# Optimization experiments

Hardware: AMD Instinct MI355X
Metric: run time of the kernel (lower is better)

The kernel has to match this reference:

```python
import jax, jax.numpy as jnp
import numpy as np

B, CH, H, W = 128, 3, 224, 224
R = 14
S = R * R  # 196 superpixels
DIMS = [11, 96, 192, 384, 768, 768]
BN_EPS = 1e-5


def setup_inputs() -> dict:
    key = jax.random.key(0)
    ks = jax.random.split(key, 64)
    inp = {}
    inp["x"] = jax.random.normal(ks[0], (B, CH, H, W), jnp.float32)
    inp["sliced"] = jax.random.randint(ks[1], (B, H, W), 0, S, jnp.int32)
    ki = 2
    for i in range(5):
        ci, co = DIMS[i], DIMS[i + 1]
        inp[f"w{i}"] = jax.random.normal(ks[ki], (co, ci), jnp.float32) / np.sqrt(ci); ki += 1
        inp[f"b{i}"] = jnp.zeros((co,), jnp.float32)
        inp[f"g{i}"] = jnp.ones((co,), jnp.float32)
        inp[f"be{i}"] = jnp.zeros((co,), jnp.float32)
        inp[f"rm{i}"] = jax.random.normal(ks[ki], (co,), jnp.float32) * 0.1; ki += 1
        inp[f"rv{i}"] = jax.random.uniform(ks[ki], (co,), jnp.float32) + 0.5; ki += 1
    return inp


def _seg_features(x, sliced):
    # x: [B,3,H,W] float, sliced: [B,H,W] int labels in [0,S)
    b, c, h, w = x.shape
    n = h * w
    ids = sliced.reshape(b, n).astype(jnp.int32)
    gid = (jnp.arange(b, dtype=jnp.int32)[:, None] * S + ids).reshape(-1)  # [B*N]

    counts = jax.ops.segment_sum(jnp.ones((b * n,), x.dtype), gid, num_segments=b * S)  # [B*S]
    rows = jnp.repeat(jnp.arange(h, dtype=x.dtype), w)
    cols = jnp.tile(jnp.arange(w, dtype=x.dtype), h)
    coords = jnp.stack([rows, cols], -1)                       # [N,2]
    coords_b = jnp.broadcast_to(coords, (b, n, 2)).reshape(b * n, 2)
    coord_sum = jax.ops.segment_sum(coords_b, gid, num_segments=b * S)  # [B*S,2]

    rgb = x.reshape(b, c, n).transpose(0, 2, 1).reshape(b * n, c)       # [B*N,3]
    rgb_sum = jax.ops.segment_sum(rgb, gid, num_segments=b * S)
    rgb_sq = jax.ops.segment_sum(rgb * rgb, gid, num_segments=b * S)

    cnt = counts[:, None]
    safe = jnp.maximum(cnt, 1.0)
    mean_coord = coord_sum / safe                              # [B*S,2]
    mean_rgb = rgb_sum / safe                                  # [B*S,3]
    # torch .std is unbiased; NaN (count<=1) replaced by 0
    var = (rgb_sq - cnt * mean_rgb * mean_rgb) / jnp.maximum(cnt - 1.0, 1.0)
    std = jnp.where(cnt > 1.0, jnp.sqrt(jnp.maximum(var, 0.0)), 0.0)

    mc = mean_coord.reshape(b, S, 2)
    mr = mean_rgb.reshape(b, S, 3)
    sd = std.reshape(b, S, 3)
    # gather pixel at the (truncated) mean location of each segment
    ri = jnp.clip(mc[..., 0].astype(jnp.int32), 0, h - 1)      # [B,S]
    ci = jnp.clip(mc[..., 1].astype(jnp.int32), 0, w - 1)
    gathered = x[jnp.arange(b)[:, None], :, ri, ci]            # [B,S,3]

    feat = jnp.concatenate([mc, mr, sd, gathered], -1)         # [B,S,11]
    feat = feat * (counts.reshape(b, S, 1) > 0).astype(x.dtype)  # absent segments stay 0
    return feat.transpose(0, 2, 1).reshape(b, 11, R, R)


def _conv_bn(h, w, b, g, be, rm, rv, act):
    # 1x1 conv == channel contraction
    h = jnp.einsum('bchw,oc->bohw', h, w) + b[None, :, None, None]
    scale = g / jnp.sqrt(rv + BN_EPS)
    h = (h - rm[None, :, None, None]) * scale[None, :, None, None] + be[None, :, None, None]
    return jax.nn.relu(h) if act else h


def reference(x, sliced,
              w0, b0, g0, be0, rm0, rv0,
              w1, b1, g1, be1, rm1, rv1,
              w2, b2, g2, be2, rm2, rv2,
              w3, b3, g3, be3, rm3, rv3,
              w4, b4, g4, be4, rm4, rv4):
    params = [(w0, b0, g0, be0, rm0, rv0), (w1, b1, g1, be1, rm1, rv1),
              (w2, b2, g2, be2, rm2, rv2), (w3, b3, g3, be3, rm3, rv3),
              (w4, b4, g4, be4, rm4, rv4)]
    h = _seg_features(x, sliced)                # [B,11,14,14]
    for i, (w, b, g, be, rm, rv) in enumerate(params):
        h = _conv_bn(h, w, b, g, be, rm, rv, act=(i < 4))  # last block: BN only
    return (sliced, h)
```

## Files before the change

kernel.cpp:

```cpp
#include <hip/hip_runtime.h>
#include <hip/hip_bf16.h>

#define HW    50176
#define IMGW  224
#define SEG   196
#define NBATCH 128
#define NCOL  (NBATCH * SEG)
#define PB    14
#define CHUNK (HW / PB)
#define VCHUNK (CHUNK / 4)

typedef __attribute__((ext_vector_type(8))) short bf16x8;
typedef __attribute__((ext_vector_type(4))) float f32x4;
typedef unsigned long long u64;

static __device__ __forceinline__ ushort f2bf(float v) {
    __hip_bfloat16 h = __float2bfloat16(v);
    return *reinterpret_cast<ushort*>(&h);
}

__global__ __launch_bounds__(256) void seg_accum(const float* __restrict__ x,
                                                 const int*   __restrict__ sl,
                                                 float*       __restrict__ stats,
                                                 float*       __restrict__ outf) {
    __shared__ u64 ls[4][SEG];
    int b    = blockIdx.x / PB;
    int part = blockIdx.x % PB;
    int tid  = threadIdx.x;

    for (int i = tid; i < 4 * SEG; i += 256) (&ls[0][0])[i] = 0ull;
    __syncthreads();

    const float* xb = x + (size_t)b * 3 * HW;
    const int*   sb = sl + (size_t)b * HW;
    float4*      ob = (float4*)(outf + (size_t)b * HW);
    int v0 = part * VCHUNK;

    for (int vi = tid; vi < VCHUNK; vi += 256) {
        int vg = v0 + vi;
        int4   id4 = ((const int4*)sb)[vg];
        float4 r4  = ((const float4*)xb)[vg];
        float4 g4  = ((const float4*)(xb + HW))[vg];
        float4 b4  = ((const float4*)(xb + 2 * HW))[vg];

        ob[vg] = make_float4((float)id4.x, (float)id4.y, (float)id4.z, (float)id4.w);

        int p   = vg * 4;
        int row = p / IMGW;
        int col = p - row * IMGW;
        u64 rowbits = ((u64)1 << 48) | ((u64)(unsigned)row << 24);

#pragma unroll
        for (int q = 0; q < 4; ++q) {
            int   id = (q == 0) ? id4.x : (q == 1) ? id4.y : (q == 2) ? id4.z : id4.w;
            float r  = (q == 0) ? r4.x  : (q == 1) ? r4.y  : (q == 2) ? r4.z  : r4.w;
            float g  = (q == 0) ? g4.x  : (q == 1) ? g4.y  : (q == 2) ? g4.z  : g4.w;
            float bl = (q == 0) ? b4.x  : (q == 1) ? b4.y  : (q == 2) ? b4.z  : b4.w;

            unsigned qr  = (unsigned)fmaf(r,  8192.f, 131072.5f);
            unsigned qg  = (unsigned)fmaf(g,  8192.f, 131072.5f);
            unsigned qb  = (unsigned)fmaf(bl, 8192.f, 131072.5f);
            unsigned qr2 = (unsigned)fmaf(r * r,  2048.f, 0.5f);
            unsigned qg2 = (unsigned)fmaf(g * g,  2048.f, 0.5f);
            unsigned qb2 = (unsigned)fmaf(bl * bl, 2048.f, 0.5f);

            atomicAdd(&ls[0][id], rowbits | (unsigned)(col + q));
            atomicAdd(&ls[1][id], ((u64)qg  << 32) | qr);
            atomicAdd(&ls[2][id], ((u64)qr2 << 32) | qb);
            atomicAdd(&ls[3][id], ((u64)qb2 << 32) | qg2);
        }
    }
    __syncthreads();

    const float inv_s = 1.f / 8192.f, inv_q = 1.f / 2048.f;
    for (int i = tid; i < SEG; i += 256) {
        u64 v0p = ls[0][i];
        unsigned cnt = (unsigned)(v0p >> 48);
        if (!cnt) continue;
        float fc   = (float)cnt;
        float rows = (float)((unsigned)(v0p >> 24) & 0xFFFFFFu);
        float cols = (float)((unsigned)v0p & 0xFFFFFFu);
        u64 v1 = ls[1][i], v2 = ls[2][i], v3 = ls[3][i];
        float bias = 16.f * fc;
        float rsum = (float)(unsigned)v1         * inv_s - bias;
        float gsum = (float)(unsigned)(v1 >> 32) * inv_s - bias;
        float bsum = (float)(unsigned)v2         * inv_s - bias;
        float rsq  = (float)(unsigned)(v2 >> 32) * inv_q;
        float gsq  = (float)(unsigned)v3         * inv_q;
        float bsq  = (float)(unsigned)(v3 >> 32) * inv_q;

        size_t base = (size_t)b * SEG + i;
        atomicAdd(&stats[0 * NCOL + base], fc);
        atomicAdd(&stats[1 * NCOL + base], rows);
        atomicAdd(&stats[2 * NCOL + base], cols);
        atomicAdd(&stats[3 * NCOL + base], rsum);
        atomicAdd(&stats[4 * NCOL + base], gsum);
        atomicAdd(&stats[5 * NCOL + base], bsum);
        atomicAdd(&stats[6 * NCOL + base], rsq);
        atomicAdd(&stats[7 * NCOL + base], gsq);
        atomicAdd(&stats[8 * NCOL + base], bsq);
    }
}

__global__ __launch_bounds__(256) void convert_all(
    const float* __restrict__ s0, const float* __restrict__ s1,
    const float* __restrict__ s2, const float* __restrict__ s3,
    const float* __restrict__ s4,
    ushort* __restrict__ d0, ushort* __restrict__ d1, ushort* __restrict__ d2,
    ushort* __restrict__ d3, ushort* __restrict__ d4) {
    int blk = blockIdx.x;
    const float* src; ushort* dst; int Cout, K, Kpad, base;
    if (blk < 32)        { src = s0; dst = d0; Cout = 96;  K = 11;  Kpad = 64;  base = 0;    }
    else if (blk < 160)  { src = s1; dst = d1; Cout = 192; K = 96;  Kpad = 128; base = 32;   }
    else if (blk < 544)  { src = s2; dst = d2; Cout = 384; K = 192; Kpad = 256; base = 160;  }
    else if (blk < 1696) { src = s3; dst = d3; Cout = 768; K = 384; Kpad = 384; base = 544;  }
    else                 { src = s4; dst = d4; Cout = 768; K = 768; Kpad = 768; base = 1696; }
    int i = (blk - base) * 256 + threadIdx.x;
    int o = i / Kpad, k = i - o * Kpad;
    float v = (o < Cout && k < K) ? src[(size_t)o * K + k] : 0.f;
    dst[i] = f2bf(v);
}

#define SH_W   0
#define SH_F   16384
#define SH_A0  20480
#define SH_A1  28672

__global__ __launch_bounds__(256) void fused_l012(
    const float* __restrict__ x,
    const float* __restrict__ stats,
    const ushort* __restrict__ W0g, const ushort* __restrict__ W1g, const ushort* __restrict__ W2g,
    const float* __restrict__ bias0, const float* __restrict__ gam0, const float* __restrict__ bet0,
    const float* __restrict__ rm0,  const float* __restrict__ rv0,
    const float* __restrict__ bias1, const float* __restrict__ gam1, const float* __restrict__ bet1,
    const float* __restrict__ rm1,  const float* __restrict__ rv1,
    const float* __restrict__ bias2, const float* __restrict__ gam2, const float* __restrict__ bet2,
    const float* __restrict__ rm2,  const float* __restrict__ rv2,
    ushort* __restrict__ outA)
{
    __shared__ ushort sh[45056];
    int tid  = threadIdx.x;
    int lane = tid & 63;
    int wid  = tid >> 6;
    int mrow = lane & 15;
    int quad = lane >> 4;
    int n0   = blockIdx.x * 64;

    if (tid < 64) {
        int r = tid, n = n0 + r;
        float cnt  = stats[n];
        float safe = fmaxf(cnt, 1.f);
        float inv  = 1.f / safe;
        float fmrow = stats[1 * NCOL + n] * inv;
        float fmcol = stats[2 * NCOL + n] * inv;
        float fmr   = stats[3 * NCOL + n] * inv;
        float fmg   = stats[4 * NCOL + n] * inv;
        float fmb   = stats[5 * NCOL + n] * inv;
        float den  = fmaxf(cnt - 1.f, 1.f);
        float vr = (stats[6 * NCOL + n] - cnt * fmr * fmr) / den;
        float vg = (stats[7 * NCOL + n] - cnt * fmg * fmg) / den;
        float vb = (stats[8 * NCOL + n] - cnt * fmb * fmb) / den;
        bool  has2 = cnt > 1.f;
        float sr = has2 ? sqrtf(fmaxf(vr, 0.f)) : 0.f;
        float sg = has2 ? sqrtf(fmaxf(vg, 0.f)) : 0.f;
        float sb = has2 ? sqrtf(fmaxf(vb, 0.f)) : 0.f;
        int b = n / SEG;
        int ri = min(max((int)fmrow, 0), IMGW - 1);
        int ci = min(max((int)fmcol, 0), IMGW - 1);
        const float* xb = x + (size_t)b * 3 * HW;
        int pi = ri * IMGW + ci;
        float gr = xb[pi], gg = xb[HW + pi], gb = xb[2 * HW + pi];
        float mask = cnt > 0.f ? 1.f : 0.f;

        int rx = r & 7;
        bf16x8 v0;
        v0[0] = (short)f2bf(fmrow * mask);
        v0[1] = (short)f2bf(fmcol * mask);
        v0[2] = (short)f2bf(fmr * mask);
        v0[3] = (short)f2bf(fmg * mask);
        v0[4] = (short)f2bf(fmb * mask);
        v0[5] = (short)f2bf(sr * mask);
        v0[6] = (short)f2bf(sg * mask);
        v0[7] = (short)f2bf(sb * mask);
        *(bf16x8*)&sh[SH_F + r * 64 + (0 ^ rx) * 8] = v0;
        bf16x8 v1 = (bf16x8){0,0,0,0,0,0,0,0};
        v1[0] = (short)f2bf(gr * mask);
        v1[1] = (short)f2bf(gg * mask);
        v1[2] = (short)f2bf(gb * mask);
        *(bf16x8*)&sh[SH_F + r * 64 + (1 ^ rx) * 8] = v1;
        bf16x8 z = (bf16x8){0,0,0,0,0,0,0,0};
        for (int g = 2; g < 8; ++g)
            *(bf16x8*)&sh[SH_F + r * 64 + (g ^ rx) * 8] = z;
    }
    __syncthreads();

    auto stageW = [&](int buf, int ot, int kt, const ushort* Wg, int Kl) {
#pragma unroll
        for (int p = 0; p < 4; ++p) {
            int flat = p * 256 + tid;
            int row = flat >> 3, kg = flat & 7;
            int kgs = kg ^ (row & 7);
            const ushort* gp = Wg + (size_t)(ot * 128 + row) * Kl + kt * 64 + kgs * 8;
            __builtin_amdgcn_global_load_lds(
                (const __attribute__((address_space(1))) void*)gp,
                (__attribute__((address_space(3))) void*)&sh[SH_W + buf * 8192 + (p * 256 + wid * 64) * 8],
                16, 0, 0);
        }
    };

    auto run_layer = [&](const ushort* Wg, int KT, int OT, int aOff, int Win,
                         const float* bb, const float* gg_, const float* bbe,
                         const float* rrm, const float* rrv, int CoutL,
                         int outOff, int Wout, int toGlobal, int Kl) {
        stageW(0, 0, 0, Wg, Kl);
        asm volatile("s_waitcnt vmcnt(0)" ::: "memory");
        __builtin_amdgcn_s_barrier();

        int T = OT * KT, cur = 0, ot = 0, kt = 0;
        f32x4 acc[4][2];
        float al[2], bt[2];
        for (int t = 0; t < T; ++t) {
            if (kt == 0) {
#pragma unroll
                for (int j = 0; j < 2; ++j) {
                    acc[0][j] = (f32x4){0.f, 0.f, 0.f, 0.f};
                    acc[1][j] = (f32x4){0.f, 0.f, 0.f, 0.f};
                    acc[2][j] = (f32x4){0.f, 0.f, 0.f, 0.f};
                    acc[3][j] = (f32x4){0.f, 0.f, 0.f, 0.f};
                    int o = ot * 128 + wid * 32 + j * 16 + mrow;
                    float a = 0.f, c = 0.f;
                    if (o < CoutL) {
                        float sc = gg_[o] / sqrtf(rrv[o] + 1e-5f);
                        a = sc;
                        c = (bb[o] - rrm[o]) * sc + bbe[o];
                    }
                    al[j] = a; bt[j] = c;
                }
            }
            if (t + 1 < T) {
                int kt2 = kt + 1, ot2 = ot;
                if (kt2 == KT) { kt2 = 0; ot2 = ot + 1; }
                stageW(cur ^ 1, ot2, kt2, Wg, Kl);
            }
#pragma unroll
            for (int ks = 0; ks < 2; ++ks) {
                bf16x8 af[4], bfr[2];
                int g = kt * 8 + ks * 4 + quad;
#pragma unroll
                for (int i = 0; i < 4; ++i) {
                    int row = i * 16 + mrow;
                    int slot = (g & ~7) | ((g ^ row) & 7);
                    af[i] = *(const bf16x8*)&sh[aOff + row * Win + slot * 8];
                }
#pragma unroll
                for (int j = 0; j < 2; ++j) {
                    int wrow = wid * 32 + j * 16 + mrow;
                    int wslot = (ks * 4 + quad) ^ (wrow & 7);
                    bfr[j] = *(const bf16x8*)&sh[SH_W + cur * 8192 + wrow * 64 + wslot * 8];
                }
#pragma unroll
                for (int i = 0; i < 4; ++i)
#pragma unroll
                    for (int j = 0; j < 2; ++j)
                        acc[i][j] = __builtin_amdgcn_mfma_f32_16x16x32_bf16(af[i], bfr[j], acc[i][j], 0, 0, 0);
            }
            if (t + 1 < T) {
                asm volatile("s_waitcnt vmcnt(0)" ::: "memory");
                __builtin_amdgcn_s_barrier();
            }
            if (kt == KT - 1) {
#pragma unroll
                for (int j = 0; j < 2; ++j) {
                    int o = ot * 128 + wid * 32 + j * 16 + mrow;
#pragma unroll
                    for (int i = 0; i < 4; ++i)
#pragma unroll
                        for (int rr = 0; rr < 4; ++rr) {
                            float v = fmaxf(acc[i][j][rr] * al[j] + bt[j], 0.f);
                            int row = i * 16 + quad * 4 + rr;
                            if (toGlobal) {
                                outA[(size_t)(n0 + row) * 384 + o] = f2bf(v);
                            } else {
                                int cg = o >> 3;
                                int slot = (cg & ~7) | ((cg ^ row) & 7);
                                sh[outOff + row * Wout + slot * 8 + (o & 7)] = f2bf(v);
                            }
                        }
                }
                kt = 0; ++ot;
            } else ++kt;
            cur ^= 1;
        }
        __syncthreads();
    };

    run_layer(W0g, 1, 1, SH_F,  64,  bias0, gam0, bet0, rm0, rv0,  96, SH_A0, 128, 0, 64);
    run_layer(W1g, 2, 2, SH_A0, 128, bias1, gam1, bet1, rm1, rv1, 192, SH_A1, 256, 0, 128);
    run_layer(W2g, 4, 3, SH_A1, 256, bias2, gam2, bet2, rm2, rv2, 384, 0,     384, 1, 256);
}

__global__ __launch_bounds__(256) void gemm_mfma(const ushort* __restrict__ Aact,
                                                 const ushort* __restrict__ Wb,
                                                 void* __restrict__ outp,
                                                 const float* __restrict__ bias,
                                                 const float* __restrict__ gam,
                                                 const float* __restrict__ bet,
                                                 const float* __restrict__ rm,
                                                 const float* __restrict__ rv,
                                                 int Kpad, int Cout, int OutStride,
                                                 int act, int final_out) {
    __shared__ ushort As[128 * 64];
    __shared__ ushort Bs[128 * 64];

    int tid  = threadIdx.x;
    int lane = tid & 63;
    int wid  = tid >> 6;
    int wm   = wid & 1;
    int wn   = wid >> 1;
    int n0   = blockIdx.x * 128;
    int o0   = blockIdx.y * 128;
    int mrow = lane & 15;
    int quad = lane >> 4;
    int swz  = mrow & 7;

    f32x4 acc[4][4];
#pragma unroll
    for (int i = 0; i < 4; ++i)
#pragma unroll
        for (int j = 0; j < 4; ++j) acc[i][j] = (f32x4){0.f, 0.f, 0.f, 0.f};

    int ktiles = Kpad >> 6;
    for (int kt = 0; kt < ktiles; ++kt) {
        int kb = kt * 64;
#pragma unroll
        for (int p = 0; p < 4; ++p) {
            int flat = p * 256 + tid;
            int row = flat >> 3, kg = flat & 7;
            int kgs = kg ^ (row & 7);
            const ushort* gp = Aact + (size_t)(n0 + row) * Kpad + kb + kgs * 8;
            __builtin_amdgcn_global_load_lds(
                (const __attribute__((address_space(1))) void*)gp,
                (__attribute__((address_space(3))) void*)(As + (size_t)(p * 256 + wid * 64) * 8),
                16, 0, 0);
        }
#pragma unroll
        for (int p = 0; p < 4; ++p) {
            int flat = p * 256 + tid;
            int row = flat >> 3, kg = flat & 7;
            int kgs = kg ^ (row & 7);
            const ushort* gp = Wb + (size_t)(o0 + row) * Kpad + kb + kgs * 8;
            __builtin_amdgcn_global_load_lds(
                (const __attribute__((address_space(1))) void*)gp,
                (__attribute__((address_space(3))) void*)(Bs + (size_t)(p * 256 + wid * 64) * 8),
                16, 0, 0);
        }
        __syncthreads();

#pragma unroll
        for (int ks = 0; ks < 2; ++ks) {
            bf16x8 af[4], bfr[4];
            int gbase = ks * 4 + quad;
            int slot  = (gbase ^ swz) * 8;
#pragma unroll
            for (int i = 0; i < 4; ++i)
                af[i] = *(const bf16x8*)&As[(size_t)(wm * 64 + i * 16 + mrow) * 64 + slot];
#pragma unroll
            for (int j = 0; j < 4; ++j)
                bfr[j] = *(const bf16x8*)&Bs[(size_t)(wn * 64 + j * 16 + mrow) * 64 + slot];
#pragma unroll
            for (int i = 0; i < 4; ++i)
#pragma unroll
                for (int j = 0; j < 4; ++j)
                    acc[i][j] = __builtin_amdgcn_mfma_f32_16x16x32_bf16(af[i], bfr[j], acc[i][j], 0, 0, 0);
        }
        __syncthreads();
    }

#pragma unroll
    for (int j = 0; j < 4; ++j) {
        int o = o0 + wn * 64 + j * 16 + mrow;
        float al = 0.f, bt = 0.f;
        if (o < Cout) {
            float sc = gam[o] / sqrtf(rv[o] + 1e-5f);
            al = sc;
            bt = (bias[o] - rm[o]) * sc + bet[o];
        }
#pragma unroll
        for (int i = 0; i < 4; ++i) {
            int nbase = n0 + wm * 64 + i * 16 + quad * 4;
#pragma unroll
            for (int r = 0; r < 4; ++r) {
                float v = acc[i][j][r] * al + bt;
                if (act) v = fmaxf(v, 0.f);
                int n = nbase + r;
                if (final_out) {
                    int b = n / SEG, s = n - b * SEG;
                    ((float*)outp)[(size_t)b * 768 * SEG + (size_t)o * SEG + s] = v;
                } else {
                    ((ushort*)outp)[(size_t)n * OutStride + o] = f2bf(v);
                }
            }
        }
    }
}

extern "C" void kernel_launch(void* const* d_in, const int* in_sizes, int n_in,
                              void* d_out, int out_size, void* d_ws, size_t ws_size,
                              hipStream_t stream) {
    const float* x  = (const float*)d_in[0];
    const int*   sl = (const int*)d_in[1];
    const float* Wp[5], *Bp[5], *Gp[5], *BEp[5], *RMp[5], *RVp[5];
    for (int i = 0; i < 5; ++i) {
        Wp[i]  = (const float*)d_in[2 + 6 * i + 0];
        Bp[i]  = (const float*)d_in[2 + 6 * i + 1];
        Gp[i]  = (const float*)d_in[2 + 6 * i + 2];
        BEp[i] = (const float*)d_in[2 + 6 * i + 3];
        RMp[i] = (const float*)d_in[2 + 6 * i + 4];
        RVp[i] = (const float*)d_in[2 + 6 * i + 5];
    }
    float* out = (float*)d_out;

    const int Kpad[5]  = {64, 128, 256, 384, 768};
    const int Cout[5]  = {96, 192, 384, 768, 768};
    const int Opad[5]  = {128, 256, 384, 768, 768};

    char* wsb = (char*)d_ws;
    float*  stats = (float*)wsb;
    wsb += (size_t)9 * NCOL * sizeof(float);
    ushort* F = (ushort*)wsb;
    wsb += (size_t)NCOL * 64 * sizeof(ushort);
    ushort* Wpad[5];
    for (int i = 0; i < 5; ++i) {
        Wpad[i] = (ushort*)wsb;
        wsb += (size_t)Opad[i] * Kpad[i] * sizeof(ushort);
    }
    ushort* bufA = (ushort*)wsb;
    wsb += (size_t)NCOL * 384 * sizeof(ushort);
    ushort* bufB = (ushort*)wsb;
    (void)F;

    hipMemsetAsync(stats, 0, (size_t)9 * NCOL * sizeof(float), stream);

    convert_all<<<4000, 256, 0, stream>>>(
        Wp[0], Wp[1], Wp[2], Wp[3], Wp[4],
        Wpad[0], Wpad[1], Wpad[2], Wpad[3], Wpad[4]);

    seg_accum<<<NBATCH * PB, 256, 0, stream>>>(x, sl, stats, out);

    fused_l012<<<NCOL / 64, 256, 0, stream>>>(
        x, stats, Wpad[0], Wpad[1], Wpad[2],
        Bp[0], Gp[0], BEp[0], RMp[0], RVp[0],
        Bp[1], Gp[1], BEp[1], RMp[1], RVp[1],
        Bp[2], Gp[2], BEp[2], RMp[2], RVp[2],
        bufA);

    const int NT = NCOL / 128;
    gemm_mfma<<<dim3(NT, Opad[3] / 128), 256, 0, stream>>>(
        bufA, Wpad[3], bufB, Bp[3], Gp[3], BEp[3], RMp[3], RVp[3],
        Kpad[3], Cout[3], Opad[3], 1, 0);
    gemm_mfma<<<dim3(NT, Opad[4] / 128), 256, 0, stream>>>(
        bufB, Wpad[4], out + (size_t)NBATCH * HW, Bp[4], Gp[4], BEp[4], RMp[4], RVp[4],
        Kpad[4], Cout[4], 0, 0, 1);
}
```

Measured before the change: 401.3 us.

## Fuse layers 3 and 4 GEMMs into one kernel keeping activations in LDS

Replaces the two separate tiled GEMM launches for layers 3 and 4 with one kernel. Each block handles 64 columns, computes the layer-3 output tile with double-buffered weight staging, and keeps the 64x768 bf16 result in shared memory as the A operand for layer 4. This removes the global round trip of the intermediate activation and one launch. The cost is 144KB of LDS per block, so occupancy drops to one block per CU. The N tile also shrinks from 128 to 64, and every block re-streams all weights.

```diff
diff --git a/kernel.cpp b/kernel.cpp
--- a/kernel.cpp
+++ b/kernel.cpp
@@ -299,107 +299,195 @@
     run_layer(W2g, 4, 3, SH_A1, 256, bias2, gam2, bet2, rm2, rv2, 384, 0,     384, 1, 256);
 }
 
-__global__ __launch_bounds__(256) void gemm_mfma(const ushort* __restrict__ Aact,
-                                                 const ushort* __restrict__ Wb,
-                                                 void* __restrict__ outp,
-                                                 const float* __restrict__ bias,
-                                                 const float* __restrict__ gam,
-                                                 const float* __restrict__ bet,
-                                                 const float* __restrict__ rm,
-                                                 const float* __restrict__ rv,
-                                                 int Kpad, int Cout, int OutStride,
-                                                 int act, int final_out) {
-    __shared__ ushort As[128 * 64];
-    __shared__ ushort Bs[128 * 64];
-
+#define L34_SG  0
+#define L34_OUT 24576
+
+__global__ __launch_bounds__(256) void fused_l34(
+    const ushort* __restrict__ Aact,
+    const ushort* __restrict__ W3g, const ushort* __restrict__ W4g,
+    const float* __restrict__ b3, const float* __restrict__ g3, const float* __restrict__ be3,
+    const float* __restrict__ rm3, const float* __restrict__ rv3,
+    const float* __restrict__ b4, const float* __restrict__ g4, const float* __restrict__ be4,
+    const float* __restrict__ rm4, const float* __restrict__ rv4,
+    float* __restrict__ outp)
+{
+    __shared__ ushort sh[73728];
     int tid  = threadIdx.x;
     int lane = tid & 63;
     int wid  = tid >> 6;
-    int wm   = wid & 1;
-    int wn   = wid >> 1;
-    int n0   = blockIdx.x * 128;
-    int o0   = blockIdx.y * 128;
     int mrow = lane & 15;
     int quad = lane >> 4;
-    int swz  = mrow & 7;
-
-    f32x4 acc[4][4];
-#pragma unroll
-    for (int i = 0; i < 4; ++i)
-#pragma unroll
-        for (int j = 0; j < 4; ++j) acc[i][j] = (f32x4){0.f, 0.f, 0.f, 0.f};
-
-    int ktiles = Kpad >> 6;
-    for (int kt = 0; kt < ktiles; ++kt) {
-        int kb = kt * 64;
+    int n0   = blockIdx.x * 64;
+
+    auto stageA3 = [&](int buf, int kt) {
+#pragma unroll
+        for (int p = 0; p < 2; ++p) {
+            int flat = p * 256 + tid;
+            int row = flat >> 3, kg = flat & 7;
+            int kgs = kg ^ (row & 7);
+            const ushort* gp = Aact + (size_t)(n0 + row) * 384 + kt * 64 + kgs * 8;
+            __builtin_amdgcn_global_load_lds(
+                (const __attribute__((address_space(1))) void*)gp,
+                (__attribute__((address_space(3))) void*)&sh[L34_SG + buf * 12288 + (p * 256 + wid * 64) * 8],
+                16, 0, 0);
+        }
+    };
+    auto stageW = [&](int buf, int ot, int kt, const ushort* Wg, int Kl) {
 #pragma unroll
         for (int p = 0; p < 4; ++p) {
             int flat = p * 256 + tid;
             int row = flat >> 3, kg = flat & 7;
             int kgs = kg ^ (row & 7);
-            const ushort* gp = Aact + (size_t)(n0 + row) * Kpad + kb + kgs * 8;
+            const ushort* gp = Wg + (size_t)(ot * 128 + row) * Kl + kt * 64 + kgs * 8;
             __builtin_amdgcn_global_load_lds(
                 (const __attribute__((address_space(1))) void*)gp,
-                (__attribute__((address_space(3))) void*)(As + (size_t)(p * 256 + wid * 64) * 8),
+                (__attribute__((address_space(3))) void*)&sh[L34_SG + buf * 12288 + 4096 + (p * 256 + wid * 64) * 8],
                 16, 0, 0);
         }
-#pragma unroll
-        for (int p = 0; p < 4; ++p) {
-            int flat = p * 256 + tid;
-            int row = flat >> 3, kg = flat & 7;
-            int kgs = kg ^ (row & 7);
-            const ushort* gp = Wb + (size_t)(o0 + row) * Kpad + kb + kgs * 8;
-            __builtin_amdgcn_global_load_lds(
-                (const __attribute__((address_space(1))) void*)gp,
-                (__attribute__((address_space(3))) void*)(Bs + (size_t)(p * 256 + wid * 64) * 8),
-                16, 0, 0);
+    };
+
+    {
+        const int KT = 6, OT = 6, T = KT * OT;
+        stageA3(0, 0);
+        stageW(0, 0, 0, W3g, 384);
+        asm volatile("s_waitcnt vmcnt(0)" ::: "memory");
+        __builtin_amdgcn_s_barrier();
+        int cur = 0, ot = 0, kt = 0;
+        f32x4 acc[4][2];
+        float al[2], bt[2];
+        for (int t = 0; t < T; ++t) {
+            if (kt == 0) {
+#pragma unroll
+                for (int j = 0; j < 2; ++j) {
+#pragma unroll
+                    for (int i = 0; i < 4; ++i) acc[i][j] = (f32x4){0.f, 0.f, 0.f, 0.f};
+                    int o = ot * 128 + wid * 32 + j * 16 + mrow;
+                    float sc = g3[o] / sqrtf(rv3[o] + 1e-5f);
+                    al[j] = sc;
+                    bt[j] = (b3[o] - rm3[o]) * sc + be3[o];
+                }
+            }
+            if (t + 1 < T) {
+                int kt2 = kt + 1, ot2 = ot;
+                if (kt2 == KT) { kt2 = 0; ot2 = ot + 1; }
+                stageA3(cur ^ 1, kt2);
+                stageW(cur ^ 1, ot2, kt2, W3g, 384);
+            }
+#pragma unroll
+            for (int ks = 0; ks < 2; ++ks) {
+                bf16x8 af[4], bfr[2];
+                int gA = ks * 4 + quad;
+#pragma unroll
+                for (int i = 0; i < 4; ++i) {
+                    int row = i * 16 + mrow;
+                    af[i] = *(const bf16x8*)&sh[L34_SG + cur * 12288 + row * 64 + (gA ^ (row & 7)) * 8];
+                }
+#pragma unroll
+                for (int j = 0; j < 2; ++j) {
+                    int wrow = wid * 32 + j * 16 + mrow;
+                    bfr[j] = *(const bf16x8*)&sh[L34_SG + cur * 12288 + 4096 + wrow * 64 + (gA ^ (wrow & 7)) * 8];
+                }
+#pragma unroll
+                for (int i = 0; i < 4; ++i)
+#pragma unroll
+                    for (int j = 0; j < 2; ++j)
+                        acc[i][j] = __builtin_amdgcn_mfma_f32_16x16x32_bf16(af[i], bfr[j], acc[i][j], 0, 0, 0);
+            }
+            if (t + 1 < T) {
+                asm volatile("s_waitcnt vmcnt(0)" ::: "memory");
+                __builtin_amdgcn_s_barrier();
+            }
+            if (kt == KT - 1) {
+#pragma unroll
+                for (int j = 0; j < 2; ++j) {
+                    int o = ot * 128 + wid * 32 + j * 16 + mrow;
+                    int cg = o >> 3;
+#pragma unroll
+                    for (int i = 0; i < 4; ++i)
+#pragma unroll
+                        for (int rr = 0; rr < 4; ++rr) {
+                            float v = fmaxf(acc[i][j][rr] * al[j] + bt[j], 0.f);
+                            int row = i * 16 + quad * 4 + rr;
+                            int slot = (cg & ~7) | ((cg ^ row) & 7);
+                            sh[L34_OUT + row * 768 + slot * 8 + (o & 7)] = f2bf(v);
+                        }
+                }
+                kt = 0; ++ot;
+            } else ++kt;
+            cur ^= 1;
         }
         __syncthreads();
-
-#pragma unroll
-        for (int ks = 0; ks < 2; ++ks) {
-            bf16x8 af[4], bfr[4];
-            int gbase = ks * 4 + quad;
-            int slot  = (gbase ^ swz) * 8;
-#pragma unroll
-            for (int i = 0; i < 4; ++i)
-                af[i] = *(const bf16x8*)&As[(size_t)(wm * 64 + i * 16 + mrow) * 64 + slot];
-#pragma unroll
-            for (int j = 0; j < 4; ++j)
-                bfr[j] = *(const bf16x8*)&Bs[(size_t)(wn * 64 + j * 16 + mrow) * 64 + slot];
-#pragma unroll
-            for (int i = 0; i < 4; ++i)
-#pragma unroll
-                for (int j = 0; j < 4; ++j)
-                    acc[i][j] = __builtin_amdgcn_mfma_f32_16x16x32_bf16(af[i], bfr[j], acc[i][j], 0, 0, 0);
-        }
-        __syncthreads();
-    }
-
-#pragma unroll
-    for (int j = 0; j < 4; ++j) {
-        int o = o0 + wn * 64 + j * 16 + mrow;
-        float al = 0.f, bt = 0.f;
-        if (o < Cout) {
-            float sc = gam[o] / sqrtf(rv[o] + 1e-5f);
-            al = sc;
-            bt = (bias[o] - rm[o]) * sc + bet[o];
-        }
-#pragma unroll
-        for (int i = 0; i < 4; ++i) {
-            int nbase = n0 + wm * 64 + i * 16 + quad * 4;
-#pragma unroll
-            for (int r = 0; r < 4; ++r) {
-                float v = acc[i][j][r] * al + bt;
-                if (act) v = fmaxf(v, 0.f);
-                int n = nbase + r;
-                if (final_out) {
-                    int b = n / SEG, s = n - b * SEG;
-                    ((float*)outp)[(size_t)b * 768 * SEG + (size_t)o * SEG + s] = v;
-                } else {
-                    ((ushort*)outp)[(size_t)n * OutStride + o] = f2bf(v);
-                }
-            }
+    }
+
+    {
+        const int KT = 12, OT = 6, T = KT * OT;
+        stageW(0, 0, 0, W4g, 768);
+        asm volatile("s_waitcnt vmcnt(0)" ::: "memory");
+        __builtin_amdgcn_s_barrier();
+        int cur = 0, ot = 0, kt = 0;
+        f32x4 acc[4][2];
+        float al[2], bt[2];
+        for (int t = 0; t < T; ++t) {
+            if (kt == 0) {
+#pragma unroll
+                for (int j = 0; j < 2; ++j) {
+#pragma unroll
+                    for (int i = 0; i < 4; ++i) acc[i][j] = (f32x4){0.f, 0.f, 0.f, 0.f};
+                    int o = ot * 128 + wid * 32 + j * 16 + mrow;
+                    float sc = g4[o] / sqrtf(rv4[o] + 1e-5f);
+                    al[j] = sc;
+                    bt[j] = (b4[o] - rm4[o]) * sc + be4[o];
+                }
+            }
+            if (t + 1 < T) {
+                int kt2 = kt + 1, ot2 = ot;
+                if (kt2 == KT) { kt2 = 0; ot2 = ot + 1; }
+                stageW(cur ^ 1, ot2, kt2, W4g, 768);
+            }
+#pragma unroll
+            for (int ks = 0; ks < 2; ++ks) {
+                bf16x8 af[4], bfr[2];
+                int g = kt * 8 + ks * 4 + quad;
+#pragma unroll
+                for (int i = 0; i < 4; ++i) {
+                    int row = i * 16 + mrow;
+                    int slot = (g & ~7) | ((g ^ row) & 7);
+                    af[i] = *(const bf16x8*)&sh[L34_OUT + row * 768 + slot * 8];
+                }
+#pragma unroll
+                for (int j = 0; j < 2; ++j) {
+                    int wrow = wid * 32 + j * 16 + mrow;
+                    int wslot = (ks * 4 + quad) ^ (wrow & 7);
+                    bfr[j] = *(const bf16x8*)&sh[L34_SG + cur * 12288 + 4096 + wrow * 64 + wslot * 8];
+                }
+#pragma unroll
+                for (int i = 0; i < 4; ++i)
+#pragma unroll
+                    for (int j = 0; j < 2; ++j)
+                        acc[i][j] = __builtin_amdgcn_mfma_f32_16x16x32_bf16(af[i], bfr[j], acc[i][j], 0, 0, 0);
+            }
+            if (t + 1 < T) {
+                asm volatile("s_waitcnt vmcnt(0)" ::: "memory");
+                __builtin_amdgcn_s_barrier();
+            }
+            if (kt == KT - 1) {
+#pragma unroll
+                for (int j = 0; j < 2; ++j) {
+                    int o = ot * 128 + wid * 32 + j * 16 + mrow;
+#pragma unroll
+                    for (int i = 0; i < 4; ++i)
+#pragma unroll
+                        for (int rr = 0; rr < 4; ++rr) {
+                            float v = acc[i][j][rr] * al[j] + bt[j];
+                            int row = i * 16 + quad * 4 + rr;
+                            int n = n0 + row;
+                            int b = n / SEG, s = n - b * SEG;
+                            outp[(size_t)b * 768 * SEG + (size_t)o * SEG + s] = v;
+                        }
+                }
+                kt = 0; ++ot;
+            } else ++kt;
+            cur ^= 1;
         }
     }
 }
@@ -421,7 +509,6 @@
     float* out = (float*)d_out;
 
     const int Kpad[5]  = {64, 128, 256, 384, 768};
-    const int Cout[5]  = {96, 192, 384, 768, 768};
     const int Opad[5]  = {128, 256, 384, 768, 768};
 
     char* wsb = (char*)d_ws;
@@ -436,7 +523,6 @@
     }
     ushort* bufA = (ushort*)wsb;
     wsb += (size_t)NCOL * 384 * sizeof(ushort);
-    ushort* bufB = (ushort*)wsb;
     (void)F;
 
     hipMemsetAsync(stats, 0, (size_t)9 * NCOL * sizeof(float), stream);
@@ -454,11 +540,9 @@
         Bp[2], Gp[2], BEp[2], RMp[2], RVp[2],
         bufA);
 
-    const int NT = NCOL / 128;
-    gemm_mfma<<<dim3(NT, Opad[3] / 128), 256, 0, stream>>>(
-        bufA, Wpad[3], bufB, Bp[3], Gp[3], BEp[3], RMp[3], RVp[3],
-        Kpad[3], Cout[3], Opad[3], 1, 0);
-    gemm_mfma<<<dim3(NT, Opad[4] / 128), 256, 0, stream>>>(
-        bufB, Wpad[4], out + (size_t)NBATCH * HW, Bp[4], Gp[4], BEp[4], RMp[4], RVp[4],
-        Kpad[4], Cout[4], 0, 0, 1);
+    fused_l34<<<NCOL / 64, 256, 0, stream>>>(
+        bufA, Wpad[3], Wpad[4],
+        Bp[3], Gp[3], BEp[3], RMp[3], RVp[3],
+        Bp[4], Gp[4], BEp[4], RMp[4], RVp[4],
+        out + (size_t)NBATCH * HW);
 }
```

Result: slower. 490.2 us (+22.2%).
